# Kernel optimization log

Hardware: AMD Instinct MI355X
Metric: run time of the kernel (lower is better)

## Reference

```python
import jax, jax.numpy as jnp
import numpy as np

N_HEAD = 16


def setup_inputs() -> dict:
    key = jax.random.key(0)
    ks = jax.random.split(key, 5)
    B, S, D = 4, 2048, 1024
    scale = 1.0 / np.sqrt(D)
    return {
        "x": jax.random.normal(ks[0], (B, S, D), dtype=jnp.float32),
        "Wq": jax.random.normal(ks[1], (D, D), dtype=jnp.float32) * scale,
        "bq": jnp.zeros((D,), dtype=jnp.float32),
        "Wk": jax.random.normal(ks[2], (D, D), dtype=jnp.float32) * scale,
        "bk": jnp.zeros((D,), dtype=jnp.float32),
        "Wv": jax.random.normal(ks[3], (D, D), dtype=jnp.float32) * scale,
        "bv": jnp.zeros((D,), dtype=jnp.float32),
        "Wo": jax.random.normal(ks[4], (D, D), dtype=jnp.float32) * scale,
        "bo": jnp.zeros((D,), dtype=jnp.float32),
    }


def reference(x, Wq, bq, Wk, bk, Wv, bv, Wo, bo):
    B, S, D = x.shape
    H = N_HEAD
    Dh = D // H
    # projections (torch Linear == x @ W^T + b; here W stored as (in, out))
    q = (x @ Wq + bq).reshape(B, S, H, Dh).transpose(0, 2, 1, 3)  # (B,H,S,Dh)
    k = (x @ Wk + bk).reshape(B, S, H, Dh).transpose(0, 2, 1, 3)
    v = (x @ Wv + bv).reshape(B, S, H, Dh).transpose(0, 2, 1, 3)
    scores = jnp.einsum("bhsd,bhtd->bhst", q, k) / jnp.sqrt(jnp.float32(Dh))
    causal = jnp.tril(jnp.ones((S, S), dtype=bool))  # (S,S)
    scores = jnp.where(causal[None, None], scores, -jnp.inf)
    weights = jax.nn.softmax(scores, axis=-1)  # (B,H,S,S)
    attn = jnp.einsum("bhst,bhtd->bhsd", weights, v)
    attn = attn.transpose(0, 2, 1, 3).reshape(B, S, D)
    out = attn @ Wo + bo
    return out
```

## Files before the change

### kernel.cpp

```cpp
#include <hip/hip_runtime.h>
#include <hip/hip_bf16.h>


typedef __bf16 bf16x8 __attribute__((ext_vector_type(8)));
typedef float f32x4 __attribute__((ext_vector_type(4)));
typedef unsigned short u16;

__device__ __forceinline__ u16 f2b(float f) {
    __hip_bfloat16 h = __float2bfloat16(f);
    return __builtin_bit_cast(unsigned short, h);
}

__device__ __forceinline__ f32x4 mfma16(bf16x8 a, bf16x8 b, f32x4 c) {
    return __builtin_amdgcn_mfma_f32_16x16x32_bf16(a, b, c, 0, 0, 0);
}

typedef const __attribute__((address_space(1))) unsigned int* gas1_t;
typedef __attribute__((address_space(3))) unsigned int* las3_t;
__device__ __forceinline__ void gld16(const void* g, void* l) {
    __builtin_amdgcn_global_load_lds((gas1_t)g, (las3_t)l, 16, 0, 0);
}

__global__ __launch_bounds__(256) void convert_x(const float* __restrict__ x,
                                                 u16* __restrict__ xb, int n4) {
    int i = blockIdx.x * 256 + threadIdx.x;
    if (i < n4) {
        float4 v = ((const float4*)x)[i];
        ushort4 u;
        u.x = f2b(v.x); u.y = f2b(v.y); u.z = f2b(v.z); u.w = f2b(v.w);
        ((ushort4*)xb)[i] = u;
    }
}

__global__ __launch_bounds__(256) void transpose_w(const float* __restrict__ Wq,
                                                   const float* __restrict__ Wk,
                                                   const float* __restrict__ Wv,
                                                   const float* __restrict__ Wo,
                                                   u16* __restrict__ wqkvt,
                                                   u16* __restrict__ wot) {
    const int z = blockIdx.z;
    const float* src = (z == 0) ? Wq : (z == 1) ? Wk : (z == 2) ? Wv : Wo;
    u16* dst = (z == 3) ? wot : (wqkvt + (size_t)z * 1024 * 1024);
    __shared__ float tile[32][33];
    const int tx = threadIdx.x, ty = threadIdx.y;
    const int nbase = blockIdx.x * 32, kbase = blockIdx.y * 32;
    for (int j = 0; j < 4; ++j)
        tile[ty + j * 8][tx] = src[(size_t)(kbase + ty + j * 8) * 1024 + nbase + tx];
    __syncthreads();
    for (int j = 0; j < 4; ++j)
        dst[(size_t)(nbase + ty + j * 8) * 1024 + kbase + tx] = f2b(tile[tx][ty + j * 8]);
}

__global__ __launch_bounds__(256) void pack_bqkv(const float* __restrict__ bq,
                                                 const float* __restrict__ bk,
                                                 const float* __restrict__ bv,
                                                 float* __restrict__ bqkv) {
    int i = blockIdx.x * 256 + threadIdx.x;
    bqkv[i] = (i < 1024) ? bq[i] : (i < 2048) ? bk[i - 1024] : bv[i - 2048];
}

__global__ __launch_bounds__(512, 2) void gemm256(const u16* __restrict__ A,
                                                  const u16* __restrict__ Bt,
                                                  const float* __restrict__ bias,
                                                  u16* __restrict__ qkout,
                                                  u16* __restrict__ vtout,
                                                  int K) {
    const int tid = threadIdx.x;
    const int l = tid & 63;
    const int w = tid >> 6;
    const int mw2 = w >> 2;
    const int nw4 = w & 3;
    const int tileM = blockIdx.x * 256;
    const int tileN = blockIdx.y * 256;

    __shared__ u16 As[2][256 * 64];
    __shared__ u16 Bs[2][256 * 64];

    const int co0 = (((l >> 4)) ^ (l & 7)) * 8;
    const int co1 = ((4 + (l >> 4)) ^ (l & 7)) * 8;
    const int mrow = l & 15;

    const int sro = l >> 3;
    const int scg = (l & 7) ^ sro;
    const u16* aSt = A + (size_t)(tileM + w * 16 + sro) * K + scg * 8;
    const u16* bSt = Bt + (size_t)(tileN + w * 16 + sro) * K + scg * 8;

    f32x4 acc[8][4] = {};
    bf16x8 aR[4][2];
    bf16x8 bR[4][2];

    auto stage = [&](int mat, int h, int tt, int nb) {
        const size_t go = (size_t)h * 128 * K + (size_t)tt * 64;
        u16* lb = (mat ? &Bs[nb][0] : &As[nb][0]) + (h * 128 + w * 16) * 64;
        const u16* gp = (mat ? bSt : aSt) + go;
        gld16(gp, lb);
        gld16(gp + (size_t)8 * K, lb + 8 * 64);
    };
    auto loadA = [&](int mh, int buf) {
#pragma unroll
        for (int i = 0; i < 4; ++i) {
            const int r = mw2 * 128 + mh * 64 + i * 16 + mrow;
            aR[i][0] = *(const bf16x8*)&As[buf][r * 64 + co0];
            aR[i][1] = *(const bf16x8*)&As[buf][r * 64 + co1];
        }
    };
    auto loadB = [&](int nh, int buf) {
#pragma unroll
        for (int j = 0; j < 2; ++j) {
            const int r = nw4 * 64 + nh * 32 + j * 16 + mrow;
            bR[nh * 2 + j][0] = *(const bf16x8*)&Bs[buf][r * 64 + co0];
            bR[nh * 2 + j][1] = *(const bf16x8*)&Bs[buf][r * 64 + co1];
        }
    };
    auto mm = [&](int mi0, int nj0) {
        __builtin_amdgcn_s_setprio(1);
#pragma unroll
        for (int ks = 0; ks < 2; ++ks)
#pragma unroll
            for (int i = 0; i < 4; ++i)
#pragma unroll
                for (int j = 0; j < 2; ++j)
                    acc[mi0 + i][nj0 + j] =
                        mfma16(aR[i][ks], bR[nj0 + j][ks], acc[mi0 + i][nj0 + j]);
        __builtin_amdgcn_s_setprio(0);
    };

    stage(0, 0, 0, 0); stage(0, 1, 0, 0); stage(1, 0, 0, 0); stage(1, 1, 0, 0);

    const int NT = K >> 6;
    for (int t = 0; t < NT; ++t) {
        const int buf = t & 1, nb = buf ^ 1;
        const bool pf = (t + 1 < NT);
        __syncthreads();

        loadA(0, buf);
        loadB(0, buf);
        if (pf) stage(0, 0, t + 1, nb);
        mm(0, 0);
        loadB(1, buf);
        if (pf) stage(0, 1, t + 1, nb);
        mm(0, 2);
        loadA(1, buf);
        if (pf) stage(1, 0, t + 1, nb);
        mm(4, 2);
        if (pf) stage(1, 1, t + 1, nb);
        mm(4, 0);
    }

    const int rbase = (l >> 4) * 4;
#pragma unroll
    for (int i = 0; i < 8; ++i) {
#pragma unroll
        for (int j = 0; j < 4; ++j) {
            const int gm0 = tileM + mw2 * 128 + i * 16 + rbase;
            const int gn = tileN + nw4 * 64 + j * 16 + (l & 15);
            const float bv_ = bias[gn];
            const f32x4 a = acc[i][j];
            if (tileN < 2048) {
                const float qs = (tileN < 1024) ? 0.125f * 1.4426950408889634f : 1.0f;
#pragma unroll
                for (int r = 0; r < 4; ++r)
                    qkout[(size_t)(gm0 + r) * 2048 + gn] = f2b((a[r] + bv_) * qs);
            } else {
                const int b = gm0 >> 11, s0 = gm0 & 2047;
                const int gn2 = gn - 2048;
                const int h = gn2 >> 6, dh = gn2 & 63;
                ushort4 u;
                u.x = f2b(a[0] + bv_); u.y = f2b(a[1] + bv_);
                u.z = f2b(a[2] + bv_); u.w = f2b(a[3] + bv_);
                *(ushort4*)&vtout[((size_t)((b * 16 + h) * 64 + dh)) * 2048 + s0] = u;
            }
        }
    }
}

template <int MODE>
__global__ __launch_bounds__(256, 2) void gemm_bt(const u16* __restrict__ A,
                                                  const u16* __restrict__ Bt,
                                                  const float* __restrict__ bias,
                                                  void* __restrict__ Cout,
                                                  void* __restrict__ Cout2,
                                                  int M, int N, int K, int ldc) {
    const int tid = threadIdx.x;
    const int l = tid & 63;
    const int w = tid >> 6;
    const int tileM = blockIdx.x * 128;
    const int tileN = blockIdx.y * 128;

    __shared__ u16 As[2][128 * 32];
    __shared__ u16 Bs[2][128 * 32];

    const int srow = l >> 2;
    const int schunk = l & 3;
    const int mrow = l & 15;
    const int g8 = (l >> 4) * 8;
    const int waveM = (w & 1) * 64;
    const int waveN = (w >> 1) * 64;

    const u16* a0 = A + (size_t)(tileM + w * 32 + srow) * K + schunk * 8;
    const u16* a1 = A + (size_t)(tileM + w * 32 + 16 + srow) * K + schunk * 8;
    const u16* b0 = Bt + (size_t)(tileN + w * 32 + srow) * K + schunk * 8;
    const u16* b1 = Bt + (size_t)(tileN + w * 32 + 16 + srow) * K + schunk * 8;

    f32x4 acc[4][4] = {};

    gld16(a0, &As[0][(w * 2) * 512]);
    gld16(a1, &As[0][(w * 2 + 1) * 512]);
    gld16(b0, &Bs[0][(w * 2) * 512]);
    gld16(b1, &Bs[0][(w * 2 + 1) * 512]);
    __syncthreads();

    for (int k0 = 0; k0 < K; k0 += 32) {
        const int cur = (k0 >> 5) & 1;
        if (k0 + 32 < K) {
            const int nb = cur ^ 1;
            gld16(a0 + k0 + 32, &As[nb][(w * 2) * 512]);
            gld16(a1 + k0 + 32, &As[nb][(w * 2 + 1) * 512]);
            gld16(b0 + k0 + 32, &Bs[nb][(w * 2) * 512]);
            gld16(b1 + k0 + 32, &Bs[nb][(w * 2 + 1) * 512]);
        }

        bf16x8 af[4], bf[4];
        for (int im = 0; im < 4; ++im)
            af[im] = *(const bf16x8*)&As[cur][(waveM + im * 16 + mrow) * 32 + g8];
        for (int in = 0; in < 4; ++in)
            bf[in] = *(const bf16x8*)&Bs[cur][(waveN + in * 16 + mrow) * 32 + g8];
        for (int im = 0; im < 4; ++im)
            for (int in = 0; in < 4; ++in)
                acc[im][in] = mfma16(af[im], bf[in], acc[im][in]);
        __syncthreads();
    }

    const int rbase = (l >> 4) * 4;
    for (int im = 0; im < 4; ++im) {
        for (int in = 0; in < 4; ++in) {
            const int gm0 = tileM + waveM + im * 16 + rbase;
            const int gn = tileN + waveN + in * 16 + (l & 15);
            const float bv_ = bias[gn];
            if (MODE == 1) {
                float* out = (float*)Cout;
                for (int r = 0; r < 4; ++r)
                    out[(size_t)(gm0 + r) * ldc + gn] = acc[im][in][r] + bv_;
            } else if (tileN < 2048) {
                const float qs = (tileN < 1024) ? 0.125f * 1.4426950408889634f : 1.0f;
                u16* out = (u16*)Cout;
                for (int r = 0; r < 4; ++r)
                    out[(size_t)(gm0 + r) * 2048 + gn] = f2b((acc[im][in][r] + bv_) * qs);
            } else {
                u16* out = (u16*)Cout2;
                const int b = gm0 >> 11, s0 = gm0 & 2047;
                const int gn2 = gn - 2048;
                const int h = gn2 >> 6, dh = gn2 & 63;
                ushort4 u;
                u.x = f2b(acc[im][in][0] + bv_);
                u.y = f2b(acc[im][in][1] + bv_);
                u.z = f2b(acc[im][in][2] + bv_);
                u.w = f2b(acc[im][in][3] + bv_);
                *(ushort4*)&out[((size_t)((b * 16 + h) * 64 + dh)) * 2048 + s0] = u;
            }
        }
    }
}

__global__ __launch_bounds__(256, 2) void attn_kernel(const u16* __restrict__ qk,
                                                      const u16* __restrict__ vt,
                                                      u16* __restrict__ attn) {
    const int bh = blockIdx.x;
    const int qt = 15 - (int)blockIdx.y;
    const int b = bh >> 4, h = bh & 15;
    const int q0 = qt * 128;
    const int tid = threadIdx.x, l = tid & 63, w = tid >> 6;
    const int q = l & 15;
    const int g = l >> 4;
    const int g8 = g * 8;

    __shared__ u16 Ks[2][64 * 64];
    __shared__ u16 Vs[2][64 * 64];
    __shared__ u16 Ps[128 * 72];

    const int sr8 = l >> 3;
    const int gc = (l & 7) ^ sr8;
    const u16* kgl = qk + (size_t)(b * 2048 + w * 16 + sr8) * 2048 + 1024 + h * 64 + gc * 8;
    const u16* vgl = vt + (size_t)(bh * 64 + w * 16 + sr8) * 2048 + gc * 8;

    for (int i = 0; i < 4; ++i) {
        const int idx = i * 256 + tid;
        const int row = idx >> 3, ch = idx & 7;
        *(uint4*)&Ps[row * 72 + ch * 8] =
            *(const uint4*)&qk[(size_t)(b * 2048 + q0 + row) * 2048 + h * 64 + ch * 8];
    }
    for (int j = 0; j < 2; ++j) {
        gld16(kgl + (size_t)(j * 8) * 2048, &Ks[0][(w * 16 + j * 8) * 64]);
        gld16(vgl + (size_t)(j * 8) * 2048, &Vs[0][(w * 16 + j * 8) * 64]);
    }
    __syncthreads();

    bf16x8 qb[2][2];
    for (int c = 0; c < 2; ++c) {
        qb[c][0] = *(const bf16x8*)&Ps[(w * 32 + c * 16 + q) * 72 + g8];
        qb[c][1] = *(const bf16x8*)&Ps[(w * 32 + c * 16 + q) * 72 + 32 + g8];
    }

    const int cl0 = ((g) ^ (q & 7)) * 8;
    const int cl1 = ((4 + g) ^ (q & 7)) * 8;

    float li[2] = {0.f, 0.f};
    f32x4 o[2][4] = {};
    const int tmax = 2 * qt + 1;
    const int tdiag = (q0 + w * 32 + 31) >> 6;

    for (int t = 0; t <= tmax; ++t) {
        const int tp = (t < tmax) ? t + 1 : tmax;
        const int nb = (t + 1) & 1;
        for (int j = 0; j < 2; ++j) {
            gld16(kgl + (size_t)(tp * 64 + j * 8) * 2048, &Ks[nb][(w * 16 + j * 8) * 64]);
            gld16(vgl + (size_t)(j * 8) * 2048 + tp * 64, &Vs[nb][(w * 16 + j * 8) * 64]);
        }

        if (t <= tdiag) {
            const int cb0 = t & 1;
            const int kv0 = t * 64;
            const u16* ks = &Ks[cb0][0];
            const u16* vs = &Vs[cb0][0];

            f32x4 st[2][4] = {};
            for (int cb = 0; cb < 4; ++cb) {
                bf16x8 ka0 = *(const bf16x8*)&ks[(cb * 16 + q) * 64 + cl0];
                bf16x8 ka1 = *(const bf16x8*)&ks[(cb * 16 + q) * 64 + cl1];
                st[0][cb] = mfma16(ka0, qb[0][0], st[0][cb]);
                st[1][cb] = mfma16(ka0, qb[1][0], st[1][cb]);
                st[0][cb] = mfma16(ka1, qb[0][1], st[0][cb]);
                st[1][cb] = mfma16(ka1, qb[1][1], st[1][cb]);
            }
            for (int c = 0; c < 2; ++c) {
                if (t == tdiag) {
                    const int qg = q0 + w * 32 + c * 16 + q;
                    for (int cb = 0; cb < 4; ++cb)
                        for (int r = 0; r < 4; ++r) {
                            const int key = kv0 + cb * 16 + g * 4 + r;
                            if (key > qg) st[c][cb][r] = -1e30f;
                        }
                }
                float ps = 0.f;
                for (int cb = 0; cb < 4; ++cb)
                    for (int r = 0; r < 4; ++r) {
                        const float p = __builtin_amdgcn_exp2f(st[c][cb][r]);
                        st[c][cb][r] = p;
                        ps += p;
                    }
                li[c] += ps;
                for (int cb = 0; cb < 4; ++cb) {
                    ushort4 u;
                    u.x = f2b(st[c][cb][0]); u.y = f2b(st[c][cb][1]);
                    u.z = f2b(st[c][cb][2]); u.w = f2b(st[c][cb][3]);
                    *(ushort4*)&Ps[(w * 32 + c * 16 + q) * 72 + cb * 16 + g * 4] = u;
                }
            }
            __builtin_amdgcn_s_waitcnt(0xC07F);
            for (int cb = 0; cb < 4; ++cb) {
                bf16x8 va0 = *(const bf16x8*)&vs[(cb * 16 + q) * 64 + cl0];
                bf16x8 va1 = *(const bf16x8*)&vs[(cb * 16 + q) * 64 + cl1];
                bf16x8 pb00 = *(const bf16x8*)&Ps[(w * 32 + q) * 72 + g8];
                bf16x8 pb01 = *(const bf16x8*)&Ps[(w * 32 + q) * 72 + 32 + g8];
                bf16x8 pb10 = *(const bf16x8*)&Ps[(w * 32 + 16 + q) * 72 + g8];
                bf16x8 pb11 = *(const bf16x8*)&Ps[(w * 32 + 16 + q) * 72 + 32 + g8];
                o[0][cb] = mfma16(va0, pb00, o[0][cb]);
                o[1][cb] = mfma16(va0, pb10, o[1][cb]);
                o[0][cb] = mfma16(va1, pb01, o[0][cb]);
                o[1][cb] = mfma16(va1, pb11, o[1][cb]);
            }
        }
        __syncthreads();
    }

    for (int c = 0; c < 2; ++c) {
        float ps = li[c];
        ps += __shfl_xor(ps, 16);
        ps += __shfl_xor(ps, 32);
        const float inv = 1.0f / ps;
        const size_t tok = (size_t)(b * 2048 + q0 + w * 32 + c * 16 + q);
        for (int cb = 0; cb < 4; ++cb) {
            ushort4 u;
            u.x = f2b(o[c][cb][0] * inv); u.y = f2b(o[c][cb][1] * inv);
            u.z = f2b(o[c][cb][2] * inv); u.w = f2b(o[c][cb][3] * inv);
            *(ushort4*)&attn[tok * 1024 + h * 64 + cb * 16 + g * 4] = u;
        }
    }
}

extern "C" void kernel_launch(void* const* d_in, const int* in_sizes, int n_in,
                              void* d_out, int out_size, void* d_ws, size_t ws_size,
                              hipStream_t stream) {
    const float* x  = (const float*)d_in[0];
    const float* Wq = (const float*)d_in[1];
    const float* bq = (const float*)d_in[2];
    const float* Wk = (const float*)d_in[3];
    const float* bk = (const float*)d_in[4];
    const float* Wv = (const float*)d_in[5];
    const float* bv = (const float*)d_in[6];
    const float* Wo = (const float*)d_in[7];
    const float* bo = (const float*)d_in[8];
    float* out = (float*)d_out;

    char* ws = (char*)d_ws;
    size_t off = 0;
    auto alloc = [&](size_t bytes) -> void* {
        void* p = ws + off;
        off += (bytes + 255) & ~(size_t)255;
        return p;
    };
    u16*   xb    = (u16*)alloc(8192ull * 1024 * 2);
    u16*   wqkvt = (u16*)alloc(3072ull * 1024 * 2);
    u16*   wot   = (u16*)alloc(1024ull * 1024 * 2);
    float* bqkv  = (float*)alloc(3072ull * 4);
    u16*   qk    = (u16*)alloc(8192ull * 2048 * 2);
    u16*   vt    = (u16*)alloc(8192ull * 1024 * 2);
    u16*   attn  = (u16*)alloc(8192ull * 1024 * 2);

    convert_x<<<8192, 256, 0, stream>>>(x, xb, 8192 * 1024 / 4);
    transpose_w<<<dim3(32, 32, 4), dim3(32, 8), 0, stream>>>(Wq, Wk, Wv, Wo, wqkvt, wot);
    pack_bqkv<<<12, 256, 0, stream>>>(bq, bk, bv, bqkv);
    gemm256<<<dim3(32, 12), 512, 0, stream>>>(xb, wqkvt, bqkv, qk, vt, 1024);
    attn_kernel<<<dim3(64, 16), 256, 0, stream>>>(qk, vt, attn);
    gemm_bt<1><<<dim3(64, 8), 256, 0, stream>>>(attn, wot, bo, out, nullptr, 8192, 1024, 1024, 1024);
}
```

Measured before the change: 244.7 us.

## Restructure QKV GEMM into deeper prefetch pipeline with split A register buffers

The QKV projection GEMM main loop is reorganized into a finer-grained schedule. Quarter-tile global-to-LDS loads are prefetched up to two K-steps ahead, with explicit vmcnt/lgkmcnt waits and raw s_barriers in place of one __syncthreads per iteration. The A fragments are double-buffered in registers so the second A half can load while the first is still in use. Launch bounds drop to one block per SIMD, giving more registers for the extra buffers at the cost of occupancy, and the hand-written wait counts make correctness depend on exact load ordering.

New measurement: 258.9 us. 1.06x slower.

```diff
diff --git a/kernel.cpp b/kernel.cpp
--- a/kernel.cpp
+++ b/kernel.cpp
@@ -59,7 +59,7 @@
     bqkv[i] = (i < 1024) ? bq[i] : (i < 2048) ? bk[i - 1024] : bv[i - 2048];
 }
 
-__global__ __launch_bounds__(512, 2) void gemm256(const u16* __restrict__ A,
+__global__ __launch_bounds__(512, 1) void gemm256(const u16* __restrict__ A,
                                                   const u16* __restrict__ Bt,
                                                   const float* __restrict__ bias,
                                                   u16* __restrict__ qkout,
@@ -86,7 +86,7 @@
     const u16* bSt = Bt + (size_t)(tileN + w * 16 + sro) * K + scg * 8;
 
     f32x4 acc[8][4] = {};
-    bf16x8 aR[4][2];
+    bf16x8 aR0[4][2], aR1[4][2];
     bf16x8 bR[4][2];
 
     auto stage = [&](int mat, int h, int tt, int nb) {
@@ -96,12 +96,12 @@
         gld16(gp, lb);
         gld16(gp + (size_t)8 * K, lb + 8 * 64);
     };
-    auto loadA = [&](int mh, int buf) {
+    auto loadA = [&](bf16x8 (&dst)[4][2], int mh, int buf) {
 #pragma unroll
         for (int i = 0; i < 4; ++i) {
             const int r = mw2 * 128 + mh * 64 + i * 16 + mrow;
-            aR[i][0] = *(const bf16x8*)&As[buf][r * 64 + co0];
-            aR[i][1] = *(const bf16x8*)&As[buf][r * 64 + co1];
+            dst[i][0] = *(const bf16x8*)&As[buf][r * 64 + co0];
+            dst[i][1] = *(const bf16x8*)&As[buf][r * 64 + co1];
         }
     };
     auto loadB = [&](int nh, int buf) {
@@ -112,7 +112,7 @@
             bR[nh * 2 + j][1] = *(const bf16x8*)&Bs[buf][r * 64 + co1];
         }
     };
-    auto mm = [&](int mi0, int nj0) {
+    auto mmq = [&](bf16x8 (&aX)[4][2], int i0, int j0) {
         __builtin_amdgcn_s_setprio(1);
 #pragma unroll
         for (int ks = 0; ks < 2; ++ks)
@@ -120,31 +120,48 @@
             for (int i = 0; i < 4; ++i)
 #pragma unroll
                 for (int j = 0; j < 2; ++j)
-                    acc[mi0 + i][nj0 + j] =
-                        mfma16(aR[i][ks], bR[nj0 + j][ks], acc[mi0 + i][nj0 + j]);
+                    acc[i0 + i][j0 + j] =
+                        mfma16(aX[i][ks], bR[j0 + j][ks], acc[i0 + i][j0 + j]);
         __builtin_amdgcn_s_setprio(0);
     };
 
-    stage(0, 0, 0, 0); stage(0, 1, 0, 0); stage(1, 0, 0, 0); stage(1, 1, 0, 0);
+    stage(1, 0, 0, 0); stage(1, 1, 0, 0); stage(0, 0, 0, 0); stage(0, 1, 0, 0);
+    stage(1, 0, 1, 1); stage(1, 1, 1, 1); stage(0, 0, 1, 1);
+    asm volatile("s_waitcnt vmcnt(6)" ::: "memory");
+    __builtin_amdgcn_s_barrier();
 
     const int NT = K >> 6;
     for (int t = 0; t < NT; ++t) {
-        const int buf = t & 1, nb = buf ^ 1;
-        const bool pf = (t + 1 < NT);
-        __syncthreads();
-
-        loadA(0, buf);
-        loadB(0, buf);
-        if (pf) stage(0, 0, t + 1, nb);
-        mm(0, 0);
-        loadB(1, buf);
-        if (pf) stage(0, 1, t + 1, nb);
-        mm(0, 2);
-        loadA(1, buf);
-        if (pf) stage(1, 0, t + 1, nb);
-        mm(4, 2);
-        if (pf) stage(1, 1, t + 1, nb);
-        mm(4, 0);
+        const int c = t & 1, n = c ^ 1;
+        const int t1 = (t + 1 < NT) ? t + 1 : NT - 1;
+        const int t2 = (t + 2 < NT) ? t + 2 : NT - 1;
+
+        loadA(aR0, 0, c);
+        loadB(0, c);
+        loadB(1, c);
+        stage(0, 1, t1, n);
+        __builtin_amdgcn_s_barrier();
+        asm volatile("s_waitcnt lgkmcnt(0)" ::: "memory");
+        mmq(aR0, 0, 0);
+        __builtin_amdgcn_s_barrier();
+
+        loadA(aR1, 1, c);
+        stage(1, 0, t2, c);
+        __builtin_amdgcn_s_barrier();
+        asm volatile("s_waitcnt lgkmcnt(0)" ::: "memory");
+        mmq(aR1, 4, 0);
+        __builtin_amdgcn_s_barrier();
+
+        stage(1, 1, t2, c);
+        __builtin_amdgcn_s_barrier();
+        mmq(aR1, 4, 2);
+        __builtin_amdgcn_s_barrier();
+
+        stage(0, 0, t2, c);
+        asm volatile("s_waitcnt vmcnt(6)" ::: "memory");
+        __builtin_amdgcn_s_barrier();
+        mmq(aR0, 0, 2);
+        __builtin_amdgcn_s_barrier();
     }
 
     const int rbase = (l >> 4) * 4;
```

## Fuse fp32-to-bf16 conversion of x into QKV GEMM A-tile staging

Applied to the files above, without the earlier changes.

Removes the separate convert_x kernel and its bf16 buffer. The QKV GEMM now reads fp32 x directly into registers, converts it to bf16 and writes swizzled tiles to LDS, while B keeps using direct global-to-LDS loads. This saves one launch and a full write and re-read of x in bf16. In exchange the GEMM reads twice the A bytes (fp32 reads are repeated for each of 12 N-tiles), uses more registers for the in-flight prefetch, and adds conversion ALU work to the main loop.

Result: slower. 385.8 us (+57.7%).

```diff
diff --git a/kernel.cpp b/kernel.cpp
--- a/kernel.cpp
+++ b/kernel.cpp
@@ -19,17 +19,6 @@
 typedef __attribute__((address_space(3))) unsigned int* las3_t;
 __device__ __forceinline__ void gld16(const void* g, void* l) {
     __builtin_amdgcn_global_load_lds((gas1_t)g, (las3_t)l, 16, 0, 0);
-}
-
-__global__ __launch_bounds__(256) void convert_x(const float* __restrict__ x,
-                                                 u16* __restrict__ xb, int n4) {
-    int i = blockIdx.x * 256 + threadIdx.x;
-    if (i < n4) {
-        float4 v = ((const float4*)x)[i];
-        ushort4 u;
-        u.x = f2b(v.x); u.y = f2b(v.y); u.z = f2b(v.z); u.w = f2b(v.w);
-        ((ushort4*)xb)[i] = u;
-    }
 }
 
 __global__ __launch_bounds__(256) void transpose_w(const float* __restrict__ Wq,
@@ -59,7 +48,7 @@
     bqkv[i] = (i < 1024) ? bq[i] : (i < 2048) ? bk[i - 1024] : bv[i - 2048];
 }
 
-__global__ __launch_bounds__(512, 2) void gemm256(const u16* __restrict__ A,
+__global__ __launch_bounds__(512, 2) void gemm256(const float* __restrict__ A,
                                                   const u16* __restrict__ Bt,
                                                   const float* __restrict__ bias,
                                                   u16* __restrict__ qkout,
@@ -82,17 +71,38 @@
 
     const int sro = l >> 3;
     const int scg = (l & 7) ^ sro;
-    const u16* aSt = A + (size_t)(tileM + w * 16 + sro) * K + scg * 8;
     const u16* bSt = Bt + (size_t)(tileN + w * 16 + sro) * K + scg * 8;
 
     f32x4 acc[8][4] = {};
     bf16x8 aR[4][2];
     bf16x8 bR[4][2];
-
-    auto stage = [&](int mat, int h, int tt, int nb) {
-        const size_t go = (size_t)h * 128 * K + (size_t)tt * 64;
-        u16* lb = (mat ? &Bs[nb][0] : &As[nb][0]) + (h * 128 + w * 16) * 64;
-        const u16* gp = (mat ? bSt : aSt) + go;
+    float4 a0F[4], a1F[4];
+
+    auto stageAload = [&](float4 (&dst)[4], int h, int tt) {
+        const float* gp = A + (size_t)(tileM + h * 128 + w * 16 + (l >> 2)) * K +
+                          tt * 64 + (l & 3) * 16;
+#pragma unroll
+        for (int i = 0; i < 4; ++i) dst[i] = *(const float4*)(gp + i * 4);
+    };
+    auto stageAwrite = [&](const float4 (&src)[4], int h, int nb) {
+        const int rl = w * 16 + (l >> 2);
+        const int swz = (l >> 2) & 7;
+        u16* base = &As[nb][(h * 128 + rl) * 64];
+#pragma unroll
+        for (int j = 0; j < 2; ++j) {
+            const float4 s0 = src[2 * j], s1 = src[2 * j + 1];
+            uint4 pk;
+            pk.x = (unsigned)f2b(s0.x) | ((unsigned)f2b(s0.y) << 16);
+            pk.y = (unsigned)f2b(s0.z) | ((unsigned)f2b(s0.w) << 16);
+            pk.z = (unsigned)f2b(s1.x) | ((unsigned)f2b(s1.y) << 16);
+            pk.w = (unsigned)f2b(s1.z) | ((unsigned)f2b(s1.w) << 16);
+            const int cg = (l & 3) * 2 + j;
+            *(uint4*)&base[(cg ^ swz) * 8] = pk;
+        }
+    };
+    auto stageB = [&](int h, int tt, int nb) {
+        const u16* gp = bSt + (size_t)h * 128 * K + (size_t)tt * 64;
+        u16* lb = &Bs[nb][(h * 128 + w * 16) * 64];
         gld16(gp, lb);
         gld16(gp + (size_t)8 * K, lb + 8 * 64);
     };
@@ -125,7 +135,9 @@
         __builtin_amdgcn_s_setprio(0);
     };
 
-    stage(0, 0, 0, 0); stage(0, 1, 0, 0); stage(1, 0, 0, 0); stage(1, 1, 0, 0);
+    stageAload(a0F, 0, 0); stageAload(a1F, 1, 0);
+    stageAwrite(a0F, 0, 0); stageAwrite(a1F, 1, 0);
+    stageB(0, 0, 0); stageB(1, 0, 0);
 
     const int NT = K >> 6;
     for (int t = 0; t < NT; ++t) {
@@ -135,15 +147,15 @@
 
         loadA(0, buf);
         loadB(0, buf);
-        if (pf) stage(0, 0, t + 1, nb);
+        if (pf) stageAload(a0F, 0, t + 1);
         mm(0, 0);
         loadB(1, buf);
-        if (pf) stage(0, 1, t + 1, nb);
+        if (pf) stageAload(a1F, 1, t + 1);
         mm(0, 2);
         loadA(1, buf);
-        if (pf) stage(1, 0, t + 1, nb);
+        if (pf) { stageAwrite(a0F, 0, nb); stageB(0, t + 1, nb); }
         mm(4, 2);
-        if (pf) stage(1, 1, t + 1, nb);
+        if (pf) { stageAwrite(a1F, 1, nb); stageB(1, t + 1, nb); }
         mm(4, 0);
     }
 
@@ -409,7 +421,6 @@
         off += (bytes + 255) & ~(size_t)255;
         return p;
     };
-    u16*   xb    = (u16*)alloc(8192ull * 1024 * 2);
     u16*   wqkvt = (u16*)alloc(3072ull * 1024 * 2);
     u16*   wot   = (u16*)alloc(1024ull * 1024 * 2);
     float* bqkv  = (float*)alloc(3072ull * 4);
@@ -417,10 +428,9 @@
     u16*   vt    = (u16*)alloc(8192ull * 1024 * 2);
     u16*   attn  = (u16*)alloc(8192ull * 1024 * 2);
 
-    convert_x<<<8192, 256, 0, stream>>>(x, xb, 8192 * 1024 / 4);
     transpose_w<<<dim3(32, 32, 4), dim3(32, 8), 0, stream>>>(Wq, Wk, Wv, Wo, wqkvt, wot);
     pack_bqkv<<<12, 256, 0, stream>>>(bq, bk, bv, bqkv);
-    gemm256<<<dim3(32, 12), 512, 0, stream>>>(xb, wqkvt, bqkv, qk, vt, 1024);
+    gemm256<<<dim3(32, 12), 512, 0, stream>>>(x, wqkvt, bqkv, qk, vt, 1024);
     attn_kernel<<<dim3(64, 16), 256, 0, stream>>>(qk, vt, attn);
     gemm_bt<1><<<dim3(64, 8), 256, 0, stream>>>(attn, wot, bo, out, nullptr, 8192, 1024, 1024, 1024);
 }
```
